# Performance work log

Measured on AMD Instinct MI355X. Metric: run time of the kernel, lower is better.

## Reference

```python
import jax, jax.numpy as jnp
import numpy as np

N = 100_000   # nodes
E = 1_600_000 # edges per graph
D = 64        # feature width
HA = 32       # attention hidden


def setup_inputs() -> dict:
    key = jax.random.key(0)
    ks = jax.random.split(key, 20)
    inp = {}
    inp["h"] = jax.random.normal(ks[0], (N, D), jnp.float32)
    inp["e_od"] = jax.random.normal(ks[1], (E, D), jnp.float32)
    inp["e_ad"] = jax.random.normal(ks[2], (E, D), jnp.float32)
    inp["src_od"] = jax.random.randint(ks[3], (E,), 0, N)
    inp["dst_od"] = jax.random.randint(ks[4], (E,), 0, N)
    inp["src_ad"] = jax.random.randint(ks[5], (E,), 0, N)
    inp["dst_ad"] = jax.random.randint(ks[6], (E,), 0, N)
    s = 1.0 / np.sqrt(D).astype(np.float32)
    # stacked params: index 0 = OD graph, index 1 = AD graph
    inp["W_src"]  = jax.random.normal(ks[7],  (2, D, D), jnp.float32) * s
    inp["W_dst"]  = jax.random.normal(ks[8],  (2, D, D), jnp.float32) * s
    inp["W_edge"] = jax.random.normal(ks[9],  (2, D, D), jnp.float32) * s
    inp["b_msg"]  = jnp.zeros((2, D), jnp.float32)
    inp["W_self"] = jax.random.normal(ks[10], (2, D, D), jnp.float32) * s
    inp["W_agg"]  = jax.random.normal(ks[11], (2, D, D), jnp.float32) * s
    inp["b_node"] = jnp.zeros((2, D), jnp.float32)
    # Attention (Aggregate_samedim): Linear(D->HA, bias) -> tanh -> Linear(HA->1, no bias)
    inp["attn_l1_w"] = jax.random.normal(ks[12], (D, HA), jnp.float32) * s
    inp["attn_l1_b"] = jnp.zeros((HA,), jnp.float32)
    inp["attn_l2_w"] = jax.random.normal(ks[13], (HA, 1), jnp.float32) * (1.0 / np.sqrt(HA).astype(np.float32))
    return inp


def reference(h, e_od, e_ad, src_od, dst_od, src_ad, dst_ad,
              W_src, W_dst, W_edge, b_msg, W_self, W_agg, b_node,
              attn_l1_w, attn_l1_b, attn_l2_w):
    def mpnn(i, e, src, dst):
        # edge message: gather src/dst node feats, small GEMMs, relu  [E, D]
        m = jax.nn.relu(h[src] @ W_src[i] + h[dst] @ W_dst[i] + e @ W_edge[i] + b_msg[i])
        # scatter-sum to destination nodes  [N, D]
        agg = jax.ops.segment_sum(m, dst, num_segments=N)
        # node update  [N, D]
        return jax.nn.relu(h @ W_self[i] + agg @ W_agg[i] + b_node[i])

    intra = mpnn(0, e_od, src_od, dst_od)  # OD graph node states
    inter = mpnn(1, e_ad, src_ad, dst_ad)  # AD graph node states
    # Aggregate_samedim: attention over the 2-way stack
    rep = jnp.stack([intra, inter], axis=1)               # [N, 2, D]
    w = jnp.tanh(rep @ attn_l1_w + attn_l1_b) @ attn_l2_w  # [N, 2, 1]
    beta = jax.nn.softmax(w, axis=1)
    return (beta * rep).sum(axis=1)                        # [N, D]
```

## Files before the change

### kernel.cpp

```cpp
#include <hip/hip_runtime.h>
#include <hip/hip_bf16.h>

using short8  = __attribute__((ext_vector_type(8))) short;
using ushort8 = __attribute__((ext_vector_type(8))) unsigned short;
using f32x4   = __attribute__((ext_vector_type(4))) float;
using fvec4   = __attribute__((ext_vector_type(4))) float;

#define CH 8192

__device__ inline unsigned short f2bf(float x) {
  union { __hip_bfloat16 b; unsigned short u; } c;
  c.b = __float2bfloat16(x);
  return c.u;
}
__device__ inline float bf2f(unsigned short s) {
  return __uint_as_float(((unsigned int)s) << 16);
}
__device__ inline unsigned int pk2(float lo, float hi) {
  union { __hip_bfloat162 b; unsigned int u; } c;
  c.b = __float22bfloat162_rn(make_float2(lo, hi));
  return c.u;
}
__device__ inline short8 cvt8(fvec4 a, fvec4 b) {
  union { short8 s; unsigned int u[4]; } r;
  r.u[0] = pk2(a[0], a[1]);
  r.u[1] = pk2(a[2], a[3]);
  r.u[2] = pk2(b[0], b[1]);
  r.u[3] = pk2(b[2], b[3]);
  return r.s;
}

__device__ inline void gload_lds16(const void* g, void* l) {
  __builtin_amdgcn_global_load_lds(
      (const __attribute__((address_space(1))) void*)g,
      (__attribute__((address_space(3))) void*)l, 16, 0, 0);
}

__device__ inline void load_bfrags_f32(const float* __restrict__ W, short8 bfr[2][4], int lane) {
  int l15 = lane & 15, lh = lane >> 4;
#pragma unroll
  for (int ks = 0; ks < 2; ++ks)
#pragma unroll
    for (int ct = 0; ct < 4; ++ct) {
      short8 v;
#pragma unroll
      for (int i = 0; i < 8; ++i)
        v[i] = (short)f2bf(W[(ks * 32 + lh * 8 + i) * 64 + ct * 16 + l15]);
      bfr[ks][ct] = v;
    }
}

__device__ inline void load_bfrags(const unsigned short* __restrict__ Wf, short8 bfr[2][4], int lane) {
#pragma unroll
  for (int ks = 0; ks < 2; ++ks)
#pragma unroll
    for (int ct = 0; ct < 4; ++ct) {
      union { ushort8 u; short8 s; } c;
      c.u = *reinterpret_cast<const ushort8*>(Wf + (((ks * 4 + ct) << 9) + (lane << 3)));
      bfr[ks][ct] = c.s;
    }
}

struct PrepArgs {
  const float* W[10];
};

__global__ __launch_bounds__(64) void prep_w_kernel(PrepArgs pw, unsigned short* __restrict__ Wf) {
  int z = blockIdx.x;
  int lane = threadIdx.x & 63;
  short8 bfr[2][4];
  load_bfrags_f32(pw.W[z], bfr, lane);
  unsigned short* dst = Wf + (size_t)z * 4096;
#pragma unroll
  for (int ks = 0; ks < 2; ++ks)
#pragma unroll
    for (int ct = 0; ct < 4; ++ct) {
      union { short8 s; ushort8 u; } c;
      c.s = bfr[ks][ct];
      *reinterpret_cast<ushort8*>(dst + (((ks * 4 + ct) << 9) + (lane << 3))) = c.u;
    }
}

struct ProjArgs {
  unsigned short* out[6];
};

__global__ __launch_bounds__(256) void proj_all_kernel(const float* __restrict__ h,
                                                       const unsigned short* __restrict__ Wf,
                                                       ProjArgs pa, int N) {
  int z = blockIdx.y;
  int lane = threadIdx.x & 63;
  int wv = threadIdx.x >> 6;
  int rowbase = blockIdx.x * 256 + wv * 64;
  int l15 = lane & 15, lh = lane >> 4;

  short8 afr[4][2];
#pragma unroll
  for (int rt = 0; rt < 4; ++rt) {
    int row = rowbase + rt * 16 + l15;
    int rc = row < N ? row : 0;
    const fvec4* p = reinterpret_cast<const fvec4*>(h + (size_t)rc * 64);
#pragma unroll
    for (int ks = 0; ks < 2; ++ks)
      afr[rt][ks] = cvt8(p[ks * 8 + lh * 2], p[ks * 8 + lh * 2 + 1]);
  }

  short8 bfr[2][4];
  load_bfrags(Wf + (size_t)z * 4096, bfr, lane);
  unsigned short* __restrict__ out = pa.out[z];

  f32x4 acc[4][4];
#pragma unroll
  for (int rt = 0; rt < 4; ++rt)
#pragma unroll
    for (int ct = 0; ct < 4; ++ct) acc[rt][ct] = (f32x4){0.f, 0.f, 0.f, 0.f};

#pragma unroll
  for (int rt = 0; rt < 4; ++rt)
#pragma unroll
    for (int ks = 0; ks < 2; ++ks)
#pragma unroll
      for (int ct = 0; ct < 4; ++ct)
        acc[rt][ct] = __builtin_amdgcn_mfma_f32_16x16x32_bf16(afr[rt][ks], bfr[ks][ct], acc[rt][ct], 0, 0, 0);

#pragma unroll
  for (int rt = 0; rt < 4; ++rt)
#pragma unroll
    for (int rg = 0; rg < 4; ++rg) {
      int row = rowbase + rt * 16 + lh * 4 + rg;
      if (row < N) {
#pragma unroll
        for (int ct = 0; ct < 4; ++ct)
          out[(size_t)row * 64 + ct * 16 + l15] = f2bf(acc[rt][ct][rg]);
      }
    }
}

__global__ __launch_bounds__(256) void hist_kernel(const int* __restrict__ dst0, const int* __restrict__ dst1,
                                                   int* __restrict__ counts, int E, int NBK) {
  __shared__ int hcnt[2048];
  int z = blockIdx.y;
  const int* __restrict__ dst = z ? dst1 : dst0;
  int t = threadIdx.x;
  for (int i = t; i < NBK; i += 256) hcnt[i] = 0;
  __syncthreads();
  int base = blockIdx.x * CH;
#pragma unroll 4
  for (int k = 0; k < CH / 256; ++k) {
    int i = base + k * 256 + t;
    if (i < E) atomicAdd(&hcnt[dst[i] >> 6], 1);
  }
  __syncthreads();
  for (int i = t; i < NBK; i += 256) {
    int c = hcnt[i];
    if (c) atomicAdd(&counts[(size_t)z * NBK + i], c);
  }
}

__global__ __launch_bounds__(1024) void scan_kernel(const int* __restrict__ counts, int* __restrict__ cursor,
                                                    int* __restrict__ gcur, int NBK) {
  int z = blockIdx.x;
  const int* c = counts + (size_t)z * NBK;
  __shared__ int lds[1024];
  int t = threadIdx.x;
  int carry = 0;
  for (int base = 0; base < NBK; base += 1024) {
    int i = base + t;
    int v = (i < NBK) ? c[i] : 0;
    lds[t] = v;
    __syncthreads();
    for (int off = 1; off < 1024; off <<= 1) {
      int x = (t >= off) ? lds[t - off] : 0;
      __syncthreads();
      lds[t] += x;
      __syncthreads();
    }
    if (i < NBK) {
      int excl = carry + lds[t] - v;
      cursor[(size_t)z * NBK + i] = excl;
      gcur[(size_t)z * NBK + i] = excl;
    }
    carry += lds[1023];
    __syncthreads();
  }
}

__global__ __launch_bounds__(256) void scatterA_kernel(
    const int* __restrict__ src0, const int* __restrict__ dst0,
    const int* __restrict__ src1, const int* __restrict__ dst1,
    int* __restrict__ gcur, int2* __restrict__ recs0, int2* __restrict__ recs1,
    int E, int NBK) {
  __shared__ int lcnt[2048];
  int z = blockIdx.y;
  const int* __restrict__ src = z ? src1 : src0;
  const int* __restrict__ dst = z ? dst1 : dst0;
  int2* __restrict__ recs = z ? recs1 : recs0;
  int t = threadIdx.x;
  for (int i = t; i < NBK; i += 256) lcnt[i] = 0;
  __syncthreads();
  int base = blockIdx.x * CH;
#pragma unroll 4
  for (int k = 0; k < CH / 256; ++k) {
    int i = base + k * 256 + t;
    if (i < E) atomicAdd(&lcnt[dst[i] >> 6], 1);
  }
  __syncthreads();
  for (int i = t; i < NBK; i += 256) {
    int c = lcnt[i];
    lcnt[i] = c ? atomicAdd(&gcur[(size_t)z * NBK + i], c) : 0;
  }
  __syncthreads();
#pragma unroll 4
  for (int k = 0; k < CH / 256; ++k) {
    int i = base + k * 256 + t;
    if (i < E) {
      int d = dst[i], s = src[i];
      int bin = d >> 6, dl = d & 63;
      int pos = atomicAdd(&lcnt[bin], 1);
      recs[pos] = make_int2(i | (bin << 21), s | (dl << 26));
    }
  }
}

__global__ __launch_bounds__(256) void sortB_kernel(int2* __restrict__ recs0, int2* __restrict__ recs1,
                                                    const int* __restrict__ cursor,
                                                    const int* __restrict__ counts, int NBK) {
  __shared__ int cnt_lds[64];
  __shared__ int cur_lds[64];
  int z = blockIdx.y;
  int b = blockIdx.x;
  int2* __restrict__ recs = z ? recs1 : recs0;
  int start = cursor[(size_t)z * NBK + b];
  int cnt = counts[(size_t)z * NBK + b];
  int t = threadIdx.x;

  for (int cbase = 0; cbase < cnt; cbase += 2048) {
    int ccnt = min(2048, cnt - cbase);
    int2 r[8];
    int dl[8];
    if (t < 64) cnt_lds[t] = 0;
    __syncthreads();
#pragma unroll
    for (int k = 0; k < 8; ++k) {
      int idx = k * 256 + t;
      if (idx < ccnt) {
        r[k] = recs[start + cbase + idx];
        dl[k] = ((unsigned)r[k].y) >> 26;
        atomicAdd(&cnt_lds[dl[k]], 1);
      }
    }
    __syncthreads();
    if (t < 64) {
      int c = cnt_lds[t];
      int x = c;
#pragma unroll
      for (int off = 1; off < 64; off <<= 1) {
        int y = __shfl_up(x, off);
        if (t >= off) x += y;
      }
      cur_lds[t] = x - c;
    }
    __syncthreads();
#pragma unroll
    for (int k = 0; k < 8; ++k) {
      int idx = k * 256 + t;
      if (idx < ccnt) {
        int pos = atomicAdd(&cur_lds[dl[k]], 1);
        recs[start + cbase + pos] = r[k];
      }
    }
    __syncthreads();
  }
}

struct EdgeArgs {
  const float* e[2];
  const int2* recs[2];
  const unsigned short* We[2];
  const float* bmsg[2];
  const unsigned short* Ps[2];
  const unsigned short* Pd[2];
  float* agg[2];
};

__global__ __launch_bounds__(256) void edge_sorted_kernel(EdgeArgs ea, int E) {
  __shared__ float e_lds[4][32 * 64];

  int z = blockIdx.y;
  const float* __restrict__ e = ea.e[z];
  const int2* __restrict__ recs = ea.recs[z];
  const unsigned short* __restrict__ Psrc = ea.Ps[z];
  const unsigned short* __restrict__ Pdst = ea.Pd[z];
  float* __restrict__ agg = ea.agg[z];

  int lane = threadIdx.x & 63;
  int wv = threadIdx.x >> 6;
  int base = (blockIdx.x * 4 + wv) * 32;
  if (base >= E) return;
  int l15 = lane & 15, lh = lane >> 4;
  char* lbase = (char*)&e_lds[wv][0];

  int slot = base + (lane & 31);
  int el = 0, sl = 0, dl = 0;
  if (slot < E) {
    int2 rc = recs[slot];
    el = rc.x & 0x1FFFFF;
    sl = rc.y & 0x3FFFFFF;
    dl = (((rc.x >> 21) & 0x7FF) << 6) | (int)(((unsigned)rc.y) >> 26);
  }

  const float* bmsg = ea.bmsg[z];
  float bv[4];
#pragma unroll
  for (int ct = 0; ct < 4; ++ct) bv[ct] = bmsg[ct * 16 + l15];

  short8 bfr[2][4];
  load_bfrags(ea.We[z], bfr, lane);

  ushort8 aP[4], aD[4];
#pragma unroll
  for (int rt = 0; rt < 2; ++rt) {
    int sr = rt * 16 + l15;
    int hr = __shfl(sl, sr);
    int dr = __shfl(dl, sr);
    const ushort8* ps = reinterpret_cast<const ushort8*>(Psrc + ((size_t)hr << 6));
    const ushort8* pd = reinterpret_cast<const ushort8*>(Pdst + ((size_t)dr << 6));
    aP[rt * 2] = ps[lh];
    aP[rt * 2 + 1] = ps[4 + lh];
    aD[rt * 2] = pd[lh];
    aD[rt * 2 + 1] = pd[4 + lh];
  }
  __builtin_amdgcn_sched_barrier(0);

  int rgrp = lane >> 4;
#pragma unroll
  for (int i = 0; i < 8; ++i) {
    int r = i * 4 + rgrp;
    int er = __shfl(el, r);
    int c = (lane & 15) ^ (r & 7);
    gload_lds16(e + ((size_t)er << 6) + c * 4, lbase + i * 1024);
  }
  __builtin_amdgcn_sched_barrier(0);

  short8 idf[2];
#pragma unroll
  for (int half = 0; half < 2; ++half) {
    short8 v;
#pragma unroll
    for (int i = 0; i < 8; ++i)
      v[i] = (short)((lh * 8 + i == half * 16 + l15) ? 0x3F80 : 0);
    idf[half] = v;
  }

  f32x4 acc[2][4];
#pragma unroll
  for (int ct = 0; ct < 4; ++ct) {
    f32x4 bb = (f32x4){bv[ct], bv[ct], bv[ct], bv[ct]};
#pragma unroll
    for (int rt = 0; rt < 2; ++rt) acc[rt][ct] = bb;
  }

#pragma unroll
  for (int rt = 0; rt < 2; ++rt) {
    union { ushort8 u; short8 s; } aP0, aP1, aD0, aD1;
    aP0.u = aP[rt * 2];
    aP1.u = aP[rt * 2 + 1];
    aD0.u = aD[rt * 2];
    aD1.u = aD[rt * 2 + 1];
    acc[rt][0] = __builtin_amdgcn_mfma_f32_16x16x32_bf16(aP0.s, idf[0], acc[rt][0], 0, 0, 0);
    acc[rt][1] = __builtin_amdgcn_mfma_f32_16x16x32_bf16(aP0.s, idf[1], acc[rt][1], 0, 0, 0);
    acc[rt][2] = __builtin_amdgcn_mfma_f32_16x16x32_bf16(aP1.s, idf[0], acc[rt][2], 0, 0, 0);
    acc[rt][3] = __builtin_amdgcn_mfma_f32_16x16x32_bf16(aP1.s, idf[1], acc[rt][3], 0, 0, 0);
    acc[rt][0] = __builtin_amdgcn_mfma_f32_16x16x32_bf16(aD0.s, idf[0], acc[rt][0], 0, 0, 0);
    acc[rt][1] = __builtin_amdgcn_mfma_f32_16x16x32_bf16(aD0.s, idf[1], acc[rt][1], 0, 0, 0);
    acc[rt][2] = __builtin_amdgcn_mfma_f32_16x16x32_bf16(aD1.s, idf[0], acc[rt][2], 0, 0, 0);
    acc[rt][3] = __builtin_amdgcn_mfma_f32_16x16x32_bf16(aD1.s, idf[1], acc[rt][3], 0, 0, 0);
  }

  asm volatile("s_waitcnt vmcnt(0)" ::: "memory");
  __builtin_amdgcn_sched_barrier(0);

#pragma unroll
  for (int rt = 0; rt < 2; ++rt) {
    int rb = rt * 16 + l15;
    int rowbyte = rb << 8;
    int x = (rb & 7) << 4;
    fvec4 p0 = *reinterpret_cast<const fvec4*>(lbase + rowbyte + (((lh * 2) << 4) ^ x));
    fvec4 p1 = *reinterpret_cast<const fvec4*>(lbase + rowbyte + (((lh * 2 + 1) << 4) ^ x));
    fvec4 p2 = *reinterpret_cast<const fvec4*>(lbase + rowbyte + (((8 + lh * 2) << 4) ^ x));
    fvec4 p3 = *reinterpret_cast<const fvec4*>(lbase + rowbyte + (((9 + lh * 2) << 4) ^ x));
    short8 aE0 = cvt8(p0, p1);
    short8 aE1 = cvt8(p2, p3);
#pragma unroll
    for (int ct = 0; ct < 4; ++ct) {
      acc[rt][ct] = __builtin_amdgcn_mfma_f32_16x16x32_bf16(aE0, bfr[0][ct], acc[rt][ct], 0, 0, 0);
      acc[rt][ct] = __builtin_amdgcn_mfma_f32_16x16x32_bf16(aE1, bfr[1][ct], acc[rt][ct], 0, 0, 0);
    }
  }

#pragma unroll
  for (int rt = 0; rt < 2; ++rt)
#pragma unroll
    for (int ct = 0; ct < 4; ++ct)
#pragma unroll
      for (int rg = 0; rg < 4; ++rg)
        acc[rt][ct][rg] = fmaxf(acc[rt][ct][rg], 0.f);

  int dprev = __shfl_up(dl, 1);
  unsigned long long bnd = __ballot(lane > 0 && dl != dprev);
  int vrows = min(32, E - base);

  int r0 = 0;
  while (r0 < vrows) {
    unsigned long long rest = (bnd >> (r0 + 1));
    int r1 = rest ? (r0 + 1 + __builtin_ctzll(rest)) : 32;
    if (r1 > vrows) r1 = vrows;
    int dcur = __shfl(dl, r0);

    float s0 = 0.f, s1 = 0.f, s2 = 0.f, s3 = 0.f;
#pragma unroll
    for (int rt = 0; rt < 2; ++rt) {
      int rs = rt * 16;
      if (r0 <= rs && r1 >= rs + 16) {
#pragma unroll
        for (int rg = 0; rg < 4; ++rg) {
          s0 += acc[rt][0][rg];
          s1 += acc[rt][1][rg];
          s2 += acc[rt][2][rg];
          s3 += acc[rt][3][rg];
        }
      } else if (r0 < rs + 16 && r1 > rs) {
#pragma unroll
        for (int rg = 0; rg < 4; ++rg) {
          int row = rs + lh * 4 + rg;
          bool in = (row >= r0) && (row < r1);
          s0 += in ? acc[rt][0][rg] : 0.f;
          s1 += in ? acc[rt][1][rg] : 0.f;
          s2 += in ? acc[rt][2][rg] : 0.f;
          s3 += in ? acc[rt][3][rg] : 0.f;
        }
      }
    }
    s0 += __shfl_xor(s0, 16); s0 += __shfl_xor(s0, 32);
    s1 += __shfl_xor(s1, 16); s1 += __shfl_xor(s1, 32);
    s2 += __shfl_xor(s2, 16); s2 += __shfl_xor(s2, 32);
    s3 += __shfl_xor(s3, 16); s3 += __shfl_xor(s3, 32);
    float mine = (lh == 0) ? s0 : (lh == 1) ? s1 : (lh == 2) ? s2 : s3;
    atomicAdd(&agg[(size_t)dcur * 64 + lane], mine);
    r0 = r1;
  }
}

struct NodeArgs {
  const float* agg[2];
  const unsigned short* T[2];
  const float* bn[2];
  unsigned short* U[2];
};

__global__ __launch_bounds__(256) void node_kernel(const unsigned short* __restrict__ Wf,
                                                   NodeArgs na, int N) {
  int z = blockIdx.y;
  const float* __restrict__ agg = na.agg[z];
  const unsigned short* __restrict__ T = na.T[z];
  const float* __restrict__ bn = na.bn[z];
  unsigned short* __restrict__ U = na.U[z];
  int lane = threadIdx.x & 63;
  int wv = threadIdx.x >> 6;
  int rowbase = blockIdx.x * 256 + wv * 64;
  int l15 = lane & 15, lh = lane >> 4;

  short8 bfr[2][4];
  load_bfrags(Wf + (size_t)(8 + z) * 4096, bfr, lane);

  f32x4 acc[4][4];
#pragma unroll
  for (int rt = 0; rt < 4; ++rt)
#pragma unroll
    for (int ct = 0; ct < 4; ++ct) acc[rt][ct] = (f32x4){0.f, 0.f, 0.f, 0.f};

#pragma unroll
  for (int rt = 0; rt < 4; ++rt) {
    int row = rowbase + rt * 16 + l15;
    int rc = row < N ? row : 0;
    const fvec4* p = reinterpret_cast<const fvec4*>(agg + (size_t)rc * 64);
#pragma unroll
    for (int ks = 0; ks < 2; ++ks) {
      fvec4 p0 = p[ks * 8 + lh * 2], p1 = p[ks * 8 + lh * 2 + 1];
      short8 ahi = cvt8(p0, p1);
      fvec4 q0, q1;
#pragma unroll
      for (int i = 0; i < 4; ++i) {
        q0[i] = p0[i] - bf2f((unsigned short)ahi[i]);
        q1[i] = p1[i] - bf2f((unsigned short)ahi[i + 4]);
      }
      short8 alo = cvt8(q0, q1);
#pragma unroll
      for (int ct = 0; ct < 4; ++ct) {
        acc[rt][ct] = __builtin_amdgcn_mfma_f32_16x16x32_bf16(ahi, bfr[ks][ct], acc[rt][ct], 0, 0, 0);
        acc[rt][ct] = __builtin_amdgcn_mfma_f32_16x16x32_bf16(alo, bfr[ks][ct], acc[rt][ct], 0, 0, 0);
      }
    }
  }

  float bv[4];
#pragma unroll
  for (int ct = 0; ct < 4; ++ct) bv[ct] = bn[ct * 16 + l15];

#pragma unroll
  for (int rt = 0; rt < 4; ++rt)
#pragma unroll
    for (int rg = 0; rg < 4; ++rg) {
      int row = rowbase + rt * 16 + lh * 4 + rg;
      if (row < N) {
#pragma unroll
        for (int ct = 0; ct < 4; ++ct) {
          int c = ct * 16 + l15;
          float v = acc[rt][ct][rg] + bf2f(T[(size_t)row * 64 + c]) + bv[ct];
          U[(size_t)row * 64 + c] = f2bf(fmaxf(v, 0.0f));
        }
      }
    }
}

__global__ __launch_bounds__(256) void attn_kernel(
    const unsigned short* __restrict__ U0, const unsigned short* __restrict__ U1,
    const float* __restrict__ l1w, const float* __restrict__ l1b, const float* __restrict__ l2w,
    float* __restrict__ out, int N) {
  int t = threadIdx.x;
  int node = blockIdx.x * 64 + (t >> 2);
  int q = t & 3;
  if (node >= N) return;
  size_t b0 = (size_t)node * 64;

  float a0[8], a1[8];
#pragma unroll
  for (int i = 0; i < 8; ++i) { a0[i] = l1b[q * 8 + i]; a1[i] = a0[i]; }

  for (int k = 0; k < 64; ++k) {
    float u0 = bf2f(U0[b0 + k]);
    float u1 = bf2f(U1[b0 + k]);
#pragma unroll
    for (int i = 0; i < 8; ++i) {
      float w = l1w[k * 32 + q * 8 + i];
      a0[i] += u0 * w;
      a1[i] += u1 * w;
    }
  }
  float w0 = 0.f, w1 = 0.f;
#pragma unroll
  for (int i = 0; i < 8; ++i) {
    float l2 = l2w[q * 8 + i];
    w0 += tanhf(a0[i]) * l2;
    w1 += tanhf(a1[i]) * l2;
  }
  w0 += __shfl_xor(w0, 1, 4); w0 += __shfl_xor(w0, 2, 4);
  w1 += __shfl_xor(w1, 1, 4); w1 += __shfl_xor(w1, 2, 4);

  float m = fmaxf(w0, w1);
  float e0 = expf(w0 - m), e1 = expf(w1 - m);
  float inv = 1.0f / (e0 + e1);
  float be0 = e0 * inv, be1 = e1 * inv;

#pragma unroll
  for (int j = 0; j < 16; ++j) {
    int c = q * 16 + j;
    out[b0 + c] = be0 * bf2f(U0[b0 + c]) + be1 * bf2f(U1[b0 + c]);
  }
}

static inline size_t au(size_t x) { return (x + 255) & ~(size_t)255; }

extern "C" void kernel_launch(void* const* d_in, const int* in_sizes, int n_in,
                              void* d_out, int out_size, void* d_ws, size_t ws_size,
                              hipStream_t stream) {
  const float* h      = (const float*)d_in[0];
  const float* e_od   = (const float*)d_in[1];
  const float* e_ad   = (const float*)d_in[2];
  const int* src_od   = (const int*)d_in[3];
  const int* dst_od   = (const int*)d_in[4];
  const int* src_ad   = (const int*)d_in[5];
  const int* dst_ad   = (const int*)d_in[6];
  const float* W_src  = (const float*)d_in[7];
  const float* W_dst  = (const float*)d_in[8];
  const float* W_edge = (const float*)d_in[9];
  const float* b_msg  = (const float*)d_in[10];
  const float* W_self = (const float*)d_in[11];
  const float* W_agg  = (const float*)d_in[12];
  const float* b_node = (const float*)d_in[13];
  const float* l1w    = (const float*)d_in[14];
  const float* l1b    = (const float*)d_in[15];
  const float* l2w    = (const float*)d_in[16];
  float* out = (float*)d_out;

  int N = in_sizes[0] / 64;
  int E = in_sizes[1] / 64;
  int NBK = (N + 63) >> 6;

  char* ws = (char*)d_ws;
  size_t off = 0;
  int* counts = (int*)(ws + off);   off += au((size_t)2 * NBK * sizeof(int));
  float* agg0 = (float*)(ws + off); off += (size_t)N * 64 * sizeof(float);
  float* agg1 = (float*)(ws + off); off += (size_t)N * 64 * sizeof(float);
  size_t zero_bytes = off;
  int* cursor = (int*)(ws + off);   off += au((size_t)2 * NBK * sizeof(int));
  int* gcur   = (int*)(ws + off);   off += au((size_t)2 * NBK * sizeof(int));
  int2* recs0 = (int2*)(ws + off);  off += au((size_t)E * sizeof(int2));
  int2* recs1 = (int2*)(ws + off);  off += au((size_t)E * sizeof(int2));
  unsigned short* Wf = (unsigned short*)(ws + off); off += au((size_t)10 * 4096 * sizeof(unsigned short));
  size_t NP = au((size_t)N * 64 * sizeof(unsigned short));
  unsigned short* Psrc0 = (unsigned short*)(ws + off); off += NP;
  unsigned short* Pdst0 = (unsigned short*)(ws + off); off += NP;
  unsigned short* Psrc1 = (unsigned short*)(ws + off); off += NP;
  unsigned short* Pdst1 = (unsigned short*)(ws + off); off += NP;
  unsigned short* T0    = (unsigned short*)(ws + off); off += NP;
  unsigned short* T1    = (unsigned short*)(ws + off); off += NP;
  unsigned short* U0 = Psrc0;
  unsigned short* U1 = Psrc1;

  hipMemsetAsync(ws, 0, zero_bytes, stream);

  PrepArgs pw;
  pw.W[0] = W_src;         pw.W[1] = W_dst;
  pw.W[2] = W_src + 4096;  pw.W[3] = W_dst + 4096;
  pw.W[4] = W_self;        pw.W[5] = W_self + 4096;
  pw.W[6] = W_edge;        pw.W[7] = W_edge + 4096;
  pw.W[8] = W_agg;         pw.W[9] = W_agg + 4096;
  prep_w_kernel<<<10, 64, 0, stream>>>(pw, Wf);

  int nb = (N + 255) / 256;
  ProjArgs pa;
  pa.out[0] = Psrc0;
  pa.out[1] = Pdst0;
  pa.out[2] = Psrc1;
  pa.out[3] = Pdst1;
  pa.out[4] = T0;
  pa.out[5] = T1;
  proj_all_kernel<<<dim3(nb, 6), 256, 0, stream>>>(h, Wf, pa, N);

  int nch = (E + CH - 1) / CH;
  hist_kernel<<<dim3(nch, 2), 256, 0, stream>>>(dst_od, dst_ad, counts, E, NBK);
  scan_kernel<<<2, 1024, 0, stream>>>(counts, cursor, gcur, NBK);
  scatterA_kernel<<<dim3(nch, 2), 256, 0, stream>>>(src_od, dst_od, src_ad, dst_ad, gcur,
                                                    recs0, recs1, E, NBK);
  sortB_kernel<<<dim3(NBK, 2), 256, 0, stream>>>(recs0, recs1, cursor, counts, NBK);

  int tiles = (E + 31) / 32;
  int eb = (tiles + 3) / 4;
  EdgeArgs ea;
  ea.e[0] = e_od;  ea.recs[0] = recs0; ea.We[0] = Wf + 6 * 4096; ea.bmsg[0] = b_msg;
  ea.Ps[0] = Psrc0; ea.Pd[0] = Pdst0; ea.agg[0] = agg0;
  ea.e[1] = e_ad;  ea.recs[1] = recs1; ea.We[1] = Wf + 7 * 4096; ea.bmsg[1] = b_msg + 64;
  ea.Ps[1] = Psrc1; ea.Pd[1] = Pdst1; ea.agg[1] = agg1;
  edge_sorted_kernel<<<dim3(eb, 2), 256, 0, stream>>>(ea, E);

  NodeArgs na;
  na.agg[0] = agg0; na.T[0] = T0; na.bn[0] = b_node;      na.U[0] = U0;
  na.agg[1] = agg1; na.T[1] = T1; na.bn[1] = b_node + 64; na.U[1] = U1;
  node_kernel<<<dim3(nb, 2), 256, 0, stream>>>(Wf, na, N);

  attn_kernel<<<(N + 63) / 64, 256, 0, stream>>>(U0, U1, l1w, l1b, l2w, out, N);
}
```

Measured before the change: 487.5 us.

## Make edge kernel persistent with software-pipelined prefetch of next tile's gathers

Turns the edge message kernel into a grid-stride persistent loop with at most 1024 blocks per graph. Each wave prefetches the next tile's records, projected node rows and edge features into LDS while it finishes the current tile's MFMAs and scatter atomics, and raises wave priority around the MFMA blocks. The projection kernel also computes two weight matrices per block, reusing the converted h fragments and halving the grid. The pipelining adds register pressure, and the LDS reuse ordering depends on the waitcnt placement.

```diff
diff --git a/kernel.cpp b/kernel.cpp
--- a/kernel.cpp
+++ b/kernel.cpp
@@ -88,7 +88,7 @@
 __global__ __launch_bounds__(256) void proj_all_kernel(const float* __restrict__ h,
                                                        const unsigned short* __restrict__ Wf,
                                                        ProjArgs pa, int N) {
-  int z = blockIdx.y;
+  int zb = blockIdx.y * 2;
   int lane = threadIdx.x & 63;
   int wv = threadIdx.x >> 6;
   int rowbase = blockIdx.x * 256 + wv * 64;
@@ -105,35 +105,38 @@
       afr[rt][ks] = cvt8(p[ks * 8 + lh * 2], p[ks * 8 + lh * 2 + 1]);
   }
 
-  short8 bfr[2][4];
-  load_bfrags(Wf + (size_t)z * 4096, bfr, lane);
-  unsigned short* __restrict__ out = pa.out[z];
-
-  f32x4 acc[4][4];
-#pragma unroll
-  for (int rt = 0; rt < 4; ++rt)
-#pragma unroll
-    for (int ct = 0; ct < 4; ++ct) acc[rt][ct] = (f32x4){0.f, 0.f, 0.f, 0.f};
-
-#pragma unroll
-  for (int rt = 0; rt < 4; ++rt)
-#pragma unroll
-    for (int ks = 0; ks < 2; ++ks)
-#pragma unroll
-      for (int ct = 0; ct < 4; ++ct)
-        acc[rt][ct] = __builtin_amdgcn_mfma_f32_16x16x32_bf16(afr[rt][ks], bfr[ks][ct], acc[rt][ct], 0, 0, 0);
-
-#pragma unroll
-  for (int rt = 0; rt < 4; ++rt)
-#pragma unroll
-    for (int rg = 0; rg < 4; ++rg) {
-      int row = rowbase + rt * 16 + lh * 4 + rg;
-      if (row < N) {
+  for (int zi = 0; zi < 2; ++zi) {
+    int z = zb + zi;
+    short8 bfr[2][4];
+    load_bfrags(Wf + (size_t)z * 4096, bfr, lane);
+    unsigned short* __restrict__ out = pa.out[z];
+
+    f32x4 acc[4][4];
+#pragma unroll
+    for (int rt = 0; rt < 4; ++rt)
+#pragma unroll
+      for (int ct = 0; ct < 4; ++ct) acc[rt][ct] = (f32x4){0.f, 0.f, 0.f, 0.f};
+
+#pragma unroll
+    for (int rt = 0; rt < 4; ++rt)
+#pragma unroll
+      for (int ks = 0; ks < 2; ++ks)
 #pragma unroll
         for (int ct = 0; ct < 4; ++ct)
-          out[(size_t)row * 64 + ct * 16 + l15] = f2bf(acc[rt][ct][rg]);
-      }
-    }
+          acc[rt][ct] = __builtin_amdgcn_mfma_f32_16x16x32_bf16(afr[rt][ks], bfr[ks][ct], acc[rt][ct], 0, 0, 0);
+
+#pragma unroll
+    for (int rt = 0; rt < 4; ++rt)
+#pragma unroll
+      for (int rg = 0; rg < 4; ++rg) {
+        int row = rowbase + rt * 16 + lh * 4 + rg;
+        if (row < N) {
+#pragma unroll
+          for (int ct = 0; ct < 4; ++ct)
+            out[(size_t)row * 64 + ct * 16 + l15] = f2bf(acc[rt][ct][rg]);
+        }
+      }
+  }
 }
 
 __global__ __launch_bounds__(256) void hist_kernel(const int* __restrict__ dst0, const int* __restrict__ dst1,
@@ -295,19 +298,14 @@
 
   int lane = threadIdx.x & 63;
   int wv = threadIdx.x >> 6;
-  int base = (blockIdx.x * 4 + wv) * 32;
-  if (base >= E) return;
   int l15 = lane & 15, lh = lane >> 4;
+  int rgrp = lane >> 4;
   char* lbase = (char*)&e_lds[wv][0];
 
-  int slot = base + (lane & 31);
-  int el = 0, sl = 0, dl = 0;
-  if (slot < E) {
-    int2 rc = recs[slot];
-    el = rc.x & 0x1FFFFF;
-    sl = rc.y & 0x3FFFFFF;
-    dl = (((rc.x >> 21) & 0x7FF) << 6) | (int)(((unsigned)rc.y) >> 26);
-  }
+  int ntiles = (E + 31) >> 5;
+  int gw = gridDim.x * 4;
+  int t0 = blockIdx.x * 4 + wv;
+  if (t0 >= ntiles) return;
 
   const float* bmsg = ea.bmsg[z];
   float bv[4];
@@ -317,6 +315,26 @@
   short8 bfr[2][4];
   load_bfrags(ea.We[z], bfr, lane);
 
+  short8 idf[2];
+#pragma unroll
+  for (int half = 0; half < 2; ++half) {
+    short8 v;
+#pragma unroll
+    for (int i = 0; i < 8; ++i)
+      v[i] = (short)((lh * 8 + i == half * 16 + l15) ? 0x3F80 : 0);
+    idf[half] = v;
+  }
+
+  int el = 0, sl = 0, dl = 0;
+  {
+    int slot = t0 * 32 + (lane & 31);
+    if (slot < E) {
+      int2 rc = recs[slot];
+      el = rc.x & 0x1FFFFF;
+      sl = rc.y & 0x3FFFFFF;
+      dl = (((rc.x >> 21) & 0x7FF) << 6) | (int)(((unsigned)rc.y) >> 26);
+    }
+  }
   ushort8 aP[4], aD[4];
 #pragma unroll
   for (int rt = 0; rt < 2; ++rt) {
@@ -331,8 +349,6 @@
     aD[rt * 2 + 1] = pd[4 + lh];
   }
   __builtin_amdgcn_sched_barrier(0);
-
-  int rgrp = lane >> 4;
 #pragma unroll
   for (int i = 0; i < 8; ++i) {
     int r = i * 4 + rgrp;
@@ -342,112 +358,149 @@
   }
   __builtin_amdgcn_sched_barrier(0);
 
-  short8 idf[2];
-#pragma unroll
-  for (int half = 0; half < 2; ++half) {
-    short8 v;
-#pragma unroll
-    for (int i = 0; i < 8; ++i)
-      v[i] = (short)((lh * 8 + i == half * 16 + l15) ? 0x3F80 : 0);
-    idf[half] = v;
-  }
-
-  f32x4 acc[2][4];
-#pragma unroll
-  for (int ct = 0; ct < 4; ++ct) {
-    f32x4 bb = (f32x4){bv[ct], bv[ct], bv[ct], bv[ct]};
-#pragma unroll
-    for (int rt = 0; rt < 2; ++rt) acc[rt][ct] = bb;
-  }
-
-#pragma unroll
-  for (int rt = 0; rt < 2; ++rt) {
-    union { ushort8 u; short8 s; } aP0, aP1, aD0, aD1;
-    aP0.u = aP[rt * 2];
-    aP1.u = aP[rt * 2 + 1];
-    aD0.u = aD[rt * 2];
-    aD1.u = aD[rt * 2 + 1];
-    acc[rt][0] = __builtin_amdgcn_mfma_f32_16x16x32_bf16(aP0.s, idf[0], acc[rt][0], 0, 0, 0);
-    acc[rt][1] = __builtin_amdgcn_mfma_f32_16x16x32_bf16(aP0.s, idf[1], acc[rt][1], 0, 0, 0);
-    acc[rt][2] = __builtin_amdgcn_mfma_f32_16x16x32_bf16(aP1.s, idf[0], acc[rt][2], 0, 0, 0);
-    acc[rt][3] = __builtin_amdgcn_mfma_f32_16x16x32_bf16(aP1.s, idf[1], acc[rt][3], 0, 0, 0);
-    acc[rt][0] = __builtin_amdgcn_mfma_f32_16x16x32_bf16(aD0.s, idf[0], acc[rt][0], 0, 0, 0);
-    acc[rt][1] = __builtin_amdgcn_mfma_f32_16x16x32_bf16(aD0.s, idf[1], acc[rt][1], 0, 0, 0);
-    acc[rt][2] = __builtin_amdgcn_mfma_f32_16x16x32_bf16(aD1.s, idf[0], acc[rt][2], 0, 0, 0);
-    acc[rt][3] = __builtin_amdgcn_mfma_f32_16x16x32_bf16(aD1.s, idf[1], acc[rt][3], 0, 0, 0);
-  }
-
-  asm volatile("s_waitcnt vmcnt(0)" ::: "memory");
-  __builtin_amdgcn_sched_barrier(0);
-
-#pragma unroll
-  for (int rt = 0; rt < 2; ++rt) {
-    int rb = rt * 16 + l15;
-    int rowbyte = rb << 8;
-    int x = (rb & 7) << 4;
-    fvec4 p0 = *reinterpret_cast<const fvec4*>(lbase + rowbyte + (((lh * 2) << 4) ^ x));
-    fvec4 p1 = *reinterpret_cast<const fvec4*>(lbase + rowbyte + (((lh * 2 + 1) << 4) ^ x));
-    fvec4 p2 = *reinterpret_cast<const fvec4*>(lbase + rowbyte + (((8 + lh * 2) << 4) ^ x));
-    fvec4 p3 = *reinterpret_cast<const fvec4*>(lbase + rowbyte + (((9 + lh * 2) << 4) ^ x));
-    short8 aE0 = cvt8(p0, p1);
-    short8 aE1 = cvt8(p2, p3);
+  for (int t = t0; t < ntiles; t += gw) {
+    int tn = t + gw;
+    bool hn = tn < ntiles;
+    int tc = hn ? tn : t0;
+    int eln = 0, sln = 0, dln = 0;
+    {
+      int slotn = tc * 32 + (lane & 31);
+      if (slotn < E) {
+        int2 rc = recs[slotn];
+        eln = rc.x & 0x1FFFFF;
+        sln = rc.y & 0x3FFFFFF;
+        dln = (((rc.x >> 21) & 0x7FF) << 6) | (int)(((unsigned)rc.y) >> 26);
+      }
+    }
+    __builtin_amdgcn_sched_barrier(0);
+
+    f32x4 acc[2][4];
 #pragma unroll
     for (int ct = 0; ct < 4; ++ct) {
-      acc[rt][ct] = __builtin_amdgcn_mfma_f32_16x16x32_bf16(aE0, bfr[0][ct], acc[rt][ct], 0, 0, 0);
-      acc[rt][ct] = __builtin_amdgcn_mfma_f32_16x16x32_bf16(aE1, bfr[1][ct], acc[rt][ct], 0, 0, 0);
-    }
-  }
-
-#pragma unroll
-  for (int rt = 0; rt < 2; ++rt)
-#pragma unroll
-    for (int ct = 0; ct < 4; ++ct)
-#pragma unroll
-      for (int rg = 0; rg < 4; ++rg)
-        acc[rt][ct][rg] = fmaxf(acc[rt][ct][rg], 0.f);
-
-  int dprev = __shfl_up(dl, 1);
-  unsigned long long bnd = __ballot(lane > 0 && dl != dprev);
-  int vrows = min(32, E - base);
-
-  int r0 = 0;
-  while (r0 < vrows) {
-    unsigned long long rest = (bnd >> (r0 + 1));
-    int r1 = rest ? (r0 + 1 + __builtin_ctzll(rest)) : 32;
-    if (r1 > vrows) r1 = vrows;
-    int dcur = __shfl(dl, r0);
-
-    float s0 = 0.f, s1 = 0.f, s2 = 0.f, s3 = 0.f;
+      f32x4 bb = (f32x4){bv[ct], bv[ct], bv[ct], bv[ct]};
+#pragma unroll
+      for (int rt = 0; rt < 2; ++rt) acc[rt][ct] = bb;
+    }
+    __builtin_amdgcn_s_setprio(1);
 #pragma unroll
     for (int rt = 0; rt < 2; ++rt) {
-      int rs = rt * 16;
-      if (r0 <= rs && r1 >= rs + 16) {
-#pragma unroll
-        for (int rg = 0; rg < 4; ++rg) {
-          s0 += acc[rt][0][rg];
-          s1 += acc[rt][1][rg];
-          s2 += acc[rt][2][rg];
-          s3 += acc[rt][3][rg];
+      union { ushort8 u; short8 s; } aP0, aP1, aD0, aD1;
+      aP0.u = aP[rt * 2];
+      aP1.u = aP[rt * 2 + 1];
+      aD0.u = aD[rt * 2];
+      aD1.u = aD[rt * 2 + 1];
+      acc[rt][0] = __builtin_amdgcn_mfma_f32_16x16x32_bf16(aP0.s, idf[0], acc[rt][0], 0, 0, 0);
+      acc[rt][1] = __builtin_amdgcn_mfma_f32_16x16x32_bf16(aP0.s, idf[1], acc[rt][1], 0, 0, 0);
+      acc[rt][2] = __builtin_amdgcn_mfma_f32_16x16x32_bf16(aP1.s, idf[0], acc[rt][2], 0, 0, 0);
+      acc[rt][3] = __builtin_amdgcn_mfma_f32_16x16x32_bf16(aP1.s, idf[1], acc[rt][3], 0, 0, 0);
+      acc[rt][0] = __builtin_amdgcn_mfma_f32_16x16x32_bf16(aD0.s, idf[0], acc[rt][0], 0, 0, 0);
+      acc[rt][1] = __builtin_amdgcn_mfma_f32_16x16x32_bf16(aD0.s, idf[1], acc[rt][1], 0, 0, 0);
+      acc[rt][2] = __builtin_amdgcn_mfma_f32_16x16x32_bf16(aD1.s, idf[0], acc[rt][2], 0, 0, 0);
+      acc[rt][3] = __builtin_amdgcn_mfma_f32_16x16x32_bf16(aD1.s, idf[1], acc[rt][3], 0, 0, 0);
+    }
+    __builtin_amdgcn_s_setprio(0);
+
+    asm volatile("s_waitcnt vmcnt(1)" ::: "memory");
+    __builtin_amdgcn_sched_barrier(0);
+
+    __builtin_amdgcn_s_setprio(1);
+#pragma unroll
+    for (int rt = 0; rt < 2; ++rt) {
+      int rb = rt * 16 + l15;
+      int rowbyte = rb << 8;
+      int x = (rb & 7) << 4;
+      fvec4 p0 = *reinterpret_cast<const fvec4*>(lbase + rowbyte + (((lh * 2) << 4) ^ x));
+      fvec4 p1 = *reinterpret_cast<const fvec4*>(lbase + rowbyte + (((lh * 2 + 1) << 4) ^ x));
+      fvec4 p2 = *reinterpret_cast<const fvec4*>(lbase + rowbyte + (((8 + lh * 2) << 4) ^ x));
+      fvec4 p3 = *reinterpret_cast<const fvec4*>(lbase + rowbyte + (((9 + lh * 2) << 4) ^ x));
+      short8 aE0 = cvt8(p0, p1);
+      short8 aE1 = cvt8(p2, p3);
+#pragma unroll
+      for (int ct = 0; ct < 4; ++ct) {
+        acc[rt][ct] = __builtin_amdgcn_mfma_f32_16x16x32_bf16(aE0, bfr[0][ct], acc[rt][ct], 0, 0, 0);
+        acc[rt][ct] = __builtin_amdgcn_mfma_f32_16x16x32_bf16(aE1, bfr[1][ct], acc[rt][ct], 0, 0, 0);
+      }
+    }
+    __builtin_amdgcn_s_setprio(0);
+
+    asm volatile("s_waitcnt lgkmcnt(0)" ::: "memory");
+    __builtin_amdgcn_sched_barrier(0);
+
+#pragma unroll
+    for (int rt = 0; rt < 2; ++rt) {
+      int sr = rt * 16 + l15;
+      int hr = __shfl(sln, sr);
+      int dr = __shfl(dln, sr);
+      const ushort8* ps = reinterpret_cast<const ushort8*>(Psrc + ((size_t)hr << 6));
+      const ushort8* pd = reinterpret_cast<const ushort8*>(Pdst + ((size_t)dr << 6));
+      aP[rt * 2] = ps[lh];
+      aP[rt * 2 + 1] = ps[4 + lh];
+      aD[rt * 2] = pd[lh];
+      aD[rt * 2 + 1] = pd[4 + lh];
+    }
+    __builtin_amdgcn_sched_barrier(0);
+#pragma unroll
+    for (int i = 0; i < 8; ++i) {
+      int r = i * 4 + rgrp;
+      int er = __shfl(eln, r);
+      int c = (lane & 15) ^ (r & 7);
+      gload_lds16(e + ((size_t)er << 6) + c * 4, lbase + i * 1024);
+    }
+    __builtin_amdgcn_sched_barrier(0);
+
+#pragma unroll
+    for (int rt = 0; rt < 2; ++rt)
+#pragma unroll
+      for (int ct = 0; ct < 4; ++ct)
+#pragma unroll
+        for (int rg = 0; rg < 4; ++rg)
+          acc[rt][ct][rg] = fmaxf(acc[rt][ct][rg], 0.f);
+
+    int dprev = __shfl_up(dl, 1);
+    unsigned long long bnd = __ballot(lane > 0 && dl != dprev);
+    int vrows = min(32, E - t * 32);
+
+    int r0 = 0;
+    while (r0 < vrows) {
+      unsigned long long rest = (bnd >> (r0 + 1));
+      int r1 = rest ? (r0 + 1 + __builtin_ctzll(rest)) : 32;
+      if (r1 > vrows) r1 = vrows;
+      int dcur = __shfl(dl, r0);
+
+      float s0 = 0.f, s1 = 0.f, s2 = 0.f, s3 = 0.f;
+#pragma unroll
+      for (int rt = 0; rt < 2; ++rt) {
+        int rs = rt * 16;
+        if (r0 <= rs && r1 >= rs + 16) {
+#pragma unroll
+          for (int rg = 0; rg < 4; ++rg) {
+            s0 += acc[rt][0][rg];
+            s1 += acc[rt][1][rg];
+            s2 += acc[rt][2][rg];
+            s3 += acc[rt][3][rg];
+          }
+        } else if (r0 < rs + 16 && r1 > rs) {
+#pragma unroll
+          for (int rg = 0; rg < 4; ++rg) {
+            int row = rs + lh * 4 + rg;
+            bool in = (row >= r0) && (row < r1);
+            s0 += in ? acc[rt][0][rg] : 0.f;
+            s1 += in ? acc[rt][1][rg] : 0.f;
+            s2 += in ? acc[rt][2][rg] : 0.f;
+            s3 += in ? acc[rt][3][rg] : 0.f;
+          }
         }
-      } else if (r0 < rs + 16 && r1 > rs) {
-#pragma unroll
-        for (int rg = 0; rg < 4; ++rg) {
-          int row = rs + lh * 4 + rg;
-          bool in = (row >= r0) && (row < r1);
-          s0 += in ? acc[rt][0][rg] : 0.f;
-          s1 += in ? acc[rt][1][rg] : 0.f;
-          s2 += in ? acc[rt][2][rg] : 0.f;
-          s3 += in ? acc[rt][3][rg] : 0.f;
-        }
-      }
-    }
-    s0 += __shfl_xor(s0, 16); s0 += __shfl_xor(s0, 32);
-    s1 += __shfl_xor(s1, 16); s1 += __shfl_xor(s1, 32);
-    s2 += __shfl_xor(s2, 16); s2 += __shfl_xor(s2, 32);
-    s3 += __shfl_xor(s3, 16); s3 += __shfl_xor(s3, 32);
-    float mine = (lh == 0) ? s0 : (lh == 1) ? s1 : (lh == 2) ? s2 : s3;
-    atomicAdd(&agg[(size_t)dcur * 64 + lane], mine);
-    r0 = r1;
+      }
+      s0 += __shfl_xor(s0, 16); s0 += __shfl_xor(s0, 32);
+      s1 += __shfl_xor(s1, 16); s1 += __shfl_xor(s1, 32);
+      s2 += __shfl_xor(s2, 16); s2 += __shfl_xor(s2, 32);
+      s3 += __shfl_xor(s3, 16); s3 += __shfl_xor(s3, 32);
+      float mine = (lh == 0) ? s0 : (lh == 1) ? s1 : (lh == 2) ? s2 : s3;
+      atomicAdd(&agg[(size_t)dcur * 64 + lane], mine);
+      r0 = r1;
+    }
+
+    el = eln; sl = sln; dl = dln;
   }
 }
 
@@ -636,7 +689,7 @@
   pa.out[3] = Pdst1;
   pa.out[4] = T0;
   pa.out[5] = T1;
-  proj_all_kernel<<<dim3(nb, 6), 256, 0, stream>>>(h, Wf, pa, N);
+  proj_all_kernel<<<dim3(nb, 3), 256, 0, stream>>>(h, Wf, pa, N);
 
   int nch = (E + CH - 1) / CH;
   hist_kernel<<<dim3(nch, 2), 256, 0, stream>>>(dst_od, dst_ad, counts, E, NBK);
@@ -645,8 +698,8 @@
                                                     recs0, recs1, E, NBK);
   sortB_kernel<<<dim3(NBK, 2), 256, 0, stream>>>(recs0, recs1, cursor, counts, NBK);
 
-  int tiles = (E + 31) / 32;
-  int eb = (tiles + 3) / 4;
+  int ntiles = (E + 31) / 32;
+  int eb = min(1024, (ntiles + 3) / 4);
   EdgeArgs ea;
   ea.e[0] = e_od;  ea.recs[0] = recs0; ea.We[0] = Wf + 6 * 4096; ea.bmsg[0] = b_msg;
   ea.Ps[0] = Psrc0; ea.Pd[0] = Pdst0; ea.agg[0] = agg0;
```

Measured after the change: 485.5 us. About the same (-0.4%).
